# Kernel optimization log

Measured on AMD Instinct MI355X. Metric: run time of the kernel, lower is better.

Reference implementation:

```python
import jax, jax.numpy as jnp
import numpy as np

B, N, C, CD, R = 8, 16384, 32, 256, 32


def setup_inputs() -> dict:
    key = jax.random.key(0)
    ks = jax.random.split(key, 12)
    f32 = jnp.float32
    p = lambda k, shape, s=0.05: jax.random.normal(k, shape, f32) * s
    return {
        "features": jax.random.normal(ks[0], (B, C, N), f32),
        "coords": jax.random.normal(ks[1], (B, 3, N), f32),
        "condition": jax.random.normal(ks[2], (B, CD), f32),
        "conv1_w": p(ks[3], (C, C, 3, 3, 3)), "conv1_b": jnp.zeros((C,), f32),
        "gn1_g": jnp.ones((C,), f32), "gn1_b": jnp.zeros((C,), f32),
        "mod1_w": p(ks[4], (2 * C, CD)),
        "mod1_b": jnp.concatenate([jnp.ones((C,)), jnp.zeros((C,))]).astype(f32),
        "conv2_w": p(ks[5], (C, C, 3, 3, 3)), "conv2_b": jnp.zeros((C,), f32),
        "gn2_g": jnp.ones((C,), f32), "gn2_b": jnp.zeros((C,), f32),
        "mod2_w": p(ks[6], (2 * C, CD)),
        "mod2_b": jnp.concatenate([jnp.ones((C,)), jnp.zeros((C,))]).astype(f32),
        "se_w1": p(ks[7], (C // 8, C)), "se_w2": p(ks[8], (C, C // 8)),
        "pc_w": p(ks[9], (C, C)), "pc_b": jnp.zeros((C,), f32),
        "gnp_g": jnp.ones((C,), f32), "gnp_b": jnp.zeros((C,), f32),
        "modp_w": p(ks[10], (2 * C, CD)),
        "modp_b": jnp.concatenate([jnp.ones((C,)), jnp.zeros((C,))]).astype(f32),
    }


def group_norm(x, g, b, G=8, eps=1e-5):
    shape = x.shape
    xg = x.reshape(shape[0], G, -1)
    m = xg.mean(-1, keepdims=True)
    v = xg.var(-1, keepdims=True)
    xn = ((xg - m) * jax.lax.rsqrt(v + eps)).reshape(shape)
    bshape = (1, shape[1]) + (1,) * (x.ndim - 2)
    return xn * g.reshape(bshape) + b.reshape(bshape)


def adagn(x, c, g, b, mw, mb):
    # GroupNorm then scale/shift from SiLU(c) @ Linear
    x = group_norm(x, g, b)
    m = jax.nn.silu(c) @ mw.T + mb  # (B, 2C)
    scale, shift = jnp.split(m, 2, axis=1)
    bshape = (x.shape[0], x.shape[1]) + (1,) * (x.ndim - 2)
    return x * scale.reshape(bshape) + shift.reshape(bshape)


def voxelize(features, coords, r):
    # scatter-average point features into r^3 grid; coords detached as in torch
    coords = jax.lax.stop_gradient(coords)
    nc = coords - coords.mean(2, keepdims=True)
    denom = jnp.max(jnp.linalg.norm(nc, axis=1, keepdims=True), axis=2, keepdims=True) * 2.0
    nc = nc / denom + 0.5
    nc = jnp.clip(nc * r, 0, r - 1)  # (B,3,N) continuous in [0, r-1]
    vc = jnp.round(nc).astype(jnp.int32)
    idx = (vc[:, 0] * r + vc[:, 1]) * r + vc[:, 2]  # (B,N) flat voxel ids

    def per_batch(f, i):
        s = jax.ops.segment_sum(f.T, i, num_segments=r ** 3)  # (V, D)
        cnt = jax.ops.segment_sum(jnp.ones(i.shape, f.dtype), i, num_segments=r ** 3)
        return (s / jnp.maximum(cnt, 1.0)[:, None]).T.reshape(f.shape[0], r, r, r)

    vox = jax.vmap(per_batch)(features, idx)  # (B, D, r, r, r)
    return vox, nc


def devoxelize(vox, coords, r):
    # trilinear gather of voxel features back to points
    Bv, D = vox.shape[:2]
    flat = vox.reshape(Bv, D, r * r * r)
    lo = jnp.floor(coords)
    frac = coords - lo
    lo = lo.astype(jnp.int32)
    hi = jnp.minimum(lo + 1, r - 1)
    gather = jax.vmap(lambda f, i: f[:, i])  # per-batch (D,V)[:, (N,)] -> (D,N)
    out = jnp.zeros((Bv, D, coords.shape[2]), vox.dtype)
    for dx in (0, 1):
        ix = hi[:, 0] if dx else lo[:, 0]
        wx = frac[:, 0] if dx else 1.0 - frac[:, 0]
        for dy in (0, 1):
            iy = hi[:, 1] if dy else lo[:, 1]
            wy = frac[:, 1] if dy else 1.0 - frac[:, 1]
            for dz in (0, 1):
                iz = hi[:, 2] if dz else lo[:, 2]
                wz = frac[:, 2] if dz else 1.0 - frac[:, 2]
                idx = (ix * r + iy) * r + iz
                out = out + gather(flat, idx) * (wx * wy * wz)[:, None, :]
    return out


def conv3d(x, w, b):
    y = jax.lax.conv_general_dilated(x, w, (1, 1, 1), 'SAME',
                                     dimension_numbers=('NCDHW', 'OIDHW', 'NCDHW'))
    return y + b[None, :, None, None, None]


def reference(features, coords, condition, conv1_w, conv1_b, gn1_g, gn1_b, mod1_w,
              mod1_b, conv2_w, conv2_b, gn2_g, gn2_b, mod2_w, mod2_b, se_w1, se_w2,
              pc_w, pc_b, gnp_g, gnp_b, modp_w, modp_b):
    vox, nc = voxelize(features, coords, R)
    v = conv3d(vox, conv1_w, conv1_b)
    v = jax.nn.silu(adagn(v, condition, gn1_g, gn1_b, mod1_w, mod1_b))
    v = conv3d(v, conv2_w, conv2_b)
    v = adagn(v, condition, gn2_g, gn2_b, mod2_w, mod2_b)
    # SE3d squeeze-excite
    s = jax.nn.sigmoid(jax.nn.relu(v.mean((2, 3, 4)) @ se_w1.T) @ se_w2.T)
    v = v * s[:, :, None, None, None]
    vfeat = devoxelize(v, nc, R)  # (B, C, N)
    # point branch: 1x1 conv + AdaGN + SiLU
    px = jnp.einsum('bdn,od->bon', features, pc_w) + pc_b[None, :, None]
    px = jax.nn.silu(adagn(px, condition, gnp_g, gnp_b, modp_w, modp_b))
    return vfeat + px
```

## Files before the change

kernel.cpp:

```cpp
#include <hip/hip_runtime.h>
#include <math.h>

#define DEV_INLINE __device__ __forceinline__

namespace {

typedef unsigned short u16;
typedef unsigned int u32;
typedef __attribute__((ext_vector_type(8))) short short8v;
typedef __attribute__((ext_vector_type(16))) float f32x16;

constexpr int Bn = 8, Cn = 32, Nn = 16384, Rn = 32, Vn = Rn * Rn * Rn;

DEV_INLINE float siluf(float x) { return x / (1.0f + __expf(-x)); }
DEV_INLINE float bf2f(u16 u) { union { u32 i; float f; } x; x.i = (u32)u << 16; return x.f; }
DEV_INLINE u16 f2bf(float f) {
  union { float f; u32 i; } x; x.f = f;
  return (u16)((x.i + 0x7FFFu + ((x.i >> 16) & 1u)) >> 16);
}
DEV_INLINE u32 pack2(float a, float b) { return (u32)f2bf(a) | ((u32)f2bf(b) << 16); }
DEV_INLINE void unpack8(uint4 u, float* f) {
  f[0] = bf2f(u.x & 0xffff); f[1] = bf2f(u.x >> 16);
  f[2] = bf2f(u.y & 0xffff); f[3] = bf2f(u.y >> 16);
  f[4] = bf2f(u.z & 0xffff); f[5] = bf2f(u.z >> 16);
  f[6] = bf2f(u.w & 0xffff); f[7] = bf2f(u.w >> 16);
}

__global__ void k_cpart1(const float* __restrict__ coords, float* __restrict__ csum) {
  int blk = blockIdx.x;
  int b = blk >> 3, s = blk & 7;
  int t = threadIdx.x;
  const float* cb = coords + (size_t)b * 3 * Nn;
  int n0 = s * 2048;
  float sx = 0.f, sy = 0.f, sz = 0.f;
  for (int n = n0 + t; n < n0 + 2048; n += 256) {
    sx += cb[n]; sy += cb[Nn + n]; sz += cb[2 * Nn + n];
  }
  #pragma unroll
  for (int m = 1; m <= 32; m <<= 1) {
    sx += __shfl_xor(sx, m); sy += __shfl_xor(sy, m); sz += __shfl_xor(sz, m);
  }
  __shared__ float rs[3][4];
  if ((t & 63) == 0) { rs[0][t >> 6] = sx; rs[1][t >> 6] = sy; rs[2][t >> 6] = sz; }
  __syncthreads();
  if (t < 3) atomicAdd(&csum[b * 4 + t], rs[t][0] + rs[t][1] + rs[t][2] + rs[t][3]);
}

__global__ void k_cpart2(const float* __restrict__ coords, const float* __restrict__ csum,
                         int* __restrict__ cmax) {
  int blk = blockIdx.x;
  int b = blk >> 3, s = blk & 7;
  int t = threadIdx.x;
  const float* cb = coords + (size_t)b * 3 * Nn;
  const float invn = 1.0f / (float)Nn;
  float mx = csum[b * 4] * invn, my = csum[b * 4 + 1] * invn, mz = csum[b * 4 + 2] * invn;
  int n0 = s * 2048;
  float mq = 0.f;
  for (int n = n0 + t; n < n0 + 2048; n += 256) {
    float x = cb[n] - mx, y = cb[Nn + n] - my, z = cb[2 * Nn + n] - mz;
    mq = fmaxf(mq, x * x + y * y + z * z);
  }
  #pragma unroll
  for (int m = 1; m <= 32; m <<= 1) mq = fmaxf(mq, __shfl_xor(mq, m));
  __shared__ float rm[4];
  if ((t & 63) == 0) rm[t >> 6] = mq;
  __syncthreads();
  if (t == 0) {
    float v = fmaxf(fmaxf(rm[0], rm[1]), fmaxf(rm[2], rm[3]));
    atomicMax(cmax + b, __float_as_int(v));
  }
}

__global__ void k_cfinal(const float* __restrict__ coords, const float* __restrict__ csum,
                         const int* __restrict__ cmax, float* __restrict__ nc,
                         int* __restrict__ vidx, int* __restrict__ hist) {
  int i = blockIdx.x * 256 + threadIdx.x;
  int b = i >> 14, n = i & (Nn - 1);
  const float* cb = coords + (size_t)b * 3 * Nn;
  const float invn = 1.0f / (float)Nn;
  float mx = csum[b * 4] * invn, my = csum[b * 4 + 1] * invn, mz = csum[b * 4 + 2] * invn;
  float inv = 1.0f / (2.0f * sqrtf(__int_as_float(cmax[b])));
  float x = (cb[n] - mx) * inv + 0.5f;
  float y = (cb[Nn + n] - my) * inv + 0.5f;
  float z = (cb[2 * Nn + n] - mz) * inv + 0.5f;
  x = fminf(fmaxf(x * (float)Rn, 0.f), (float)(Rn - 1));
  y = fminf(fmaxf(y * (float)Rn, 0.f), (float)(Rn - 1));
  z = fminf(fmaxf(z * (float)Rn, 0.f), (float)(Rn - 1));
  float* ncb = nc + (size_t)b * 3 * Nn;
  ncb[n] = x; ncb[Nn + n] = y; ncb[2 * Nn + n] = z;
  int vx = (int)rintf(x), vy = (int)rintf(y), vz = (int)rintf(z);
  int v = (vx * Rn + vy) * Rn + vz;
  vidx[i] = v;
  atomicAdd(&hist[b * Vn + v], 1);
}

__global__ __launch_bounds__(256, 2) void k_pxlin(
    const float* __restrict__ feat, const float* __restrict__ w,
    const float* __restrict__ bias, float* __restrict__ featT,
    u16* __restrict__ pxb) {
  __shared__ float lw[1024];
  __shared__ float lb[32];
  __shared__ float lbuf[256 * 33];
  int t = threadIdx.x;
  for (int i = t; i < 1024; i += 256) lw[i] = w[i];
  if (t < 32) lb[t] = bias[t];
  int blk = blockIdx.x;
  int b = blk >> 6, tile = blk & 63;
  int n0 = tile * 256, n = n0 + t;
  float fr[32];
  const float* fb = feat + (size_t)b * 32 * Nn + n;
  #pragma unroll
  for (int ci = 0; ci < 32; ++ci) {
    fr[ci] = fb[(size_t)ci * Nn];
    lbuf[t * 33 + ci] = fr[ci];
  }
  __syncthreads();
  float* ftb = featT + ((size_t)b * Nn + n0) * 32;
  #pragma unroll
  for (int j = 0; j < 32; ++j) {
    int idx = j * 256 + t;
    ftb[idx] = lbuf[(idx >> 5) * 33 + (idx & 31)];
  }
  __syncthreads();
  u32* lbu = reinterpret_cast<u32*>(lbuf);
  #pragma unroll
  for (int p2 = 0; p2 < 16; ++p2) {
    int co0 = p2 * 2;
    float a0 = lb[co0], a1 = lb[co0 + 1];
    #pragma unroll
    for (int ci = 0; ci < 32; ++ci) {
      a0 += lw[co0 * 32 + ci] * fr[ci];
      a1 += lw[(co0 + 1) * 32 + ci] * fr[ci];
    }
    lbu[t * 17 + p2] = pack2(a0, a1);
  }
  __syncthreads();
  u32* pxu = reinterpret_cast<u32*>(pxb) + ((size_t)b * Nn + n0) * 16;
  #pragma unroll
  for (int j = 0; j < 16; ++j) {
    int idx = j * 256 + t;
    pxu[idx] = lbu[(idx >> 4) * 17 + (idx & 15)];
  }
}

__global__ void k_scan1(const int* __restrict__ hist, int* __restrict__ offs,
                        int* __restrict__ bsum) {
  __shared__ int sd[256];
  int t = threadIdx.x, blk = blockIdx.x;
  int4 h = reinterpret_cast<const int4*>(hist)[blk * 256 + t];
  int s = h.x + h.y + h.z + h.w;
  sd[t] = s; __syncthreads();
  for (int off = 1; off < 256; off <<= 1) {
    int add = (t >= off) ? sd[t - off] : 0;
    __syncthreads();
    sd[t] += add;
    __syncthreads();
  }
  int excl = sd[t] - s;
  int4 o;
  o.x = excl; o.y = excl + h.x; o.z = o.y + h.y; o.w = o.z + h.z;
  reinterpret_cast<int4*>(offs)[blk * 256 + t] = o;
  if (t == 0) bsum[blk] = sd[255];
}

__global__ void k_scan2(const int* __restrict__ bsum, int* __restrict__ bbase) {
  __shared__ int sd[256];
  int t = threadIdx.x;
  int s = bsum[t];
  sd[t] = s; __syncthreads();
  for (int off = 1; off < 256; off <<= 1) {
    int add = (t >= off) ? sd[t - off] : 0;
    __syncthreads();
    sd[t] += add;
    __syncthreads();
  }
  bbase[t] = sd[t] - s;
}

__global__ void k_sortidx(const int* __restrict__ vidx, int* __restrict__ offs,
                          const int* __restrict__ bbase, int* __restrict__ pidx) {
  int i = blockIdx.x * 256 + threadIdx.x;
  int b = i >> 14, n = i & (Nn - 1);
  int g = b * Vn + vidx[i];
  int p = atomicAdd(&offs[g], 1) + bbase[g >> 10];
  pidx[p] = n;
}

__global__ void k_voxavg(const int* __restrict__ hist, const int* __restrict__ offs,
                         const int* __restrict__ bbase, const int* __restrict__ pidx,
                         const float* __restrict__ featT, uint2* __restrict__ vox0) {
  int t = threadIdx.x;
  int wv = blockIdx.x * 4 + (t >> 6);
  int lane = t & 63;
  int c4 = lane & 7, j = lane >> 3;
  int b = wv >> 15;
  int cnt = hist[wv];
  float ax = 0.f, ay = 0.f, az = 0.f, aw = 0.f;
  if (cnt > 0) {
    int end = offs[wv] + bbase[wv >> 10];
    int start = end - cnt;
    const float4* ft = reinterpret_cast<const float4*>(featT) + (size_t)b * Nn * 8;
    for (int k = start + j; k < end; k += 8) {
      int n = pidx[k];
      float4 v = ft[n * 8 + c4];
      ax += v.x; ay += v.y; az += v.z; aw += v.w;
    }
    #pragma unroll
    for (int m = 8; m <= 32; m <<= 1) {
      ax += __shfl_xor(ax, m); ay += __shfl_xor(ay, m);
      az += __shfl_xor(az, m); aw += __shfl_xor(aw, m);
    }
    float invc = 1.0f / (float)cnt;
    ax *= invc; ay *= invc; az *= invc; aw *= invc;
  }
  if (j == 0) {
    uint2 o;
    o.x = pack2(ax, ay);
    o.y = pack2(az, aw);
    vox0[(size_t)wv * 8 + c4] = o;
  }
}

__global__ void k_twz(const float* __restrict__ w, u16* __restrict__ wt) {
  int i = blockIdx.x * 256 + threadIdx.x;
  if (i >= 27 * 32 * 32) return;
  int e = i & 7, l = (i >> 3) & 63, h = (i >> 9) & 1, k = i >> 10;
  int co = l & 31, ci = h * 16 + ((l >> 5) << 3) + e;
  wt[i] = f2bf(w[(co * 32 + ci) * 27 + k]);
}

__global__ void k_mods(const float* __restrict__ cond,
                       const float* __restrict__ w1, const float* __restrict__ b1,
                       const float* __restrict__ w2, const float* __restrict__ b2,
                       const float* __restrict__ wp, const float* __restrict__ bp,
                       float* __restrict__ m1, float* __restrict__ m2,
                       float* __restrict__ mp) {
  int blk = blockIdx.x;
  int mat = blk >> 3, b = blk & 7;
  int t = threadIdx.x;
  __shared__ float sc[256];
  sc[t] = siluf(cond[b * 256 + t]);
  __syncthreads();
  const float* w = (mat == 0) ? w1 : ((mat == 1) ? w2 : wp);
  const float* bb = (mat == 0) ? b1 : ((mat == 1) ? b2 : bp);
  float* dst = (mat == 0) ? m1 : ((mat == 1) ? m2 : mp);
  int wave = t >> 6, lane = t & 63;
  const float4* w4 = reinterpret_cast<const float4*>(w);
  float4 sv = reinterpret_cast<const float4*>(sc)[lane];
  #pragma unroll
  for (int i = 0; i < 16; ++i) {
    int oo = wave * 16 + i;
    float4 wv = w4[oo * 64 + lane];
    float p = wv.x * sv.x + wv.y * sv.y + wv.z * sv.z + wv.w * sv.w;
    #pragma unroll
    for (int m = 1; m <= 32; m <<= 1) p += __shfl_xor(p, m);
    if (lane == 0) dst[b * 64 + oo] = p + bb[oo];
  }
}

template <bool AFF>
__global__ __launch_bounds__(512, 4) void k_conv(
    const u16* __restrict__ in, const u16* __restrict__ wt,
    const float* __restrict__ bias, const float* __restrict__ Ac,
    const float* __restrict__ Bc, u16* __restrict__ out,
    float* __restrict__ pstat) {
  __shared__ uint4 lds_x4[4096];
  int t = threadIdx.x;
  int blk = blockIdx.x;
  int yp = blk & 3, x = (blk >> 2) & 31, b = blk >> 7;
  int y0 = yp * 8;
  size_t bbase = (size_t)b * Vn;

  for (int i = t; i < 4080; i += 512) {
    int col = i / 136, rem = i - col * 136;
    int c4 = rem / 34, r = rem - c4 * 34;
    int dxp = col / 10, yy = col - dxp * 10;
    int gx = x + dxp - 1, gy = y0 + yy - 1, z = r - 1;
    uint4 val = make_uint4(0u, 0u, 0u, 0u);
    if (gx >= 0 && gx < 32 && (unsigned)gy < 32u && (unsigned)z < 32u) {
      val = *reinterpret_cast<const uint4*>(
          in + (bbase + (size_t)((gx * 32 + gy) * 32 + z)) * 32 + c4 * 8);
      if (AFF) {
        float f[8];
        unpack8(val, f);
        float4 A0 = reinterpret_cast<const float4*>(Ac)[b * 8 + c4 * 2];
        float4 A1 = reinterpret_cast<const float4*>(Ac)[b * 8 + c4 * 2 + 1];
        float4 B0 = reinterpret_cast<const float4*>(Bc)[b * 8 + c4 * 2];
        float4 B1 = reinterpret_cast<const float4*>(Bc)[b * 8 + c4 * 2 + 1];
        f[0] = siluf(f[0] * A0.x + B0.x); f[1] = siluf(f[1] * A0.y + B0.y);
        f[2] = siluf(f[2] * A0.z + B0.z); f[3] = siluf(f[3] * A0.w + B0.w);
        f[4] = siluf(f[4] * A1.x + B1.x); f[5] = siluf(f[5] * A1.y + B1.y);
        f[6] = siluf(f[6] * A1.z + B1.z); f[7] = siluf(f[7] * A1.w + B1.w);
        val.x = pack2(f[0], f[1]); val.y = pack2(f[2], f[3]);
        val.z = pack2(f[4], f[5]); val.w = pack2(f[6], f[7]);
      }
    }
    lds_x4[i] = val;
  }
  __syncthreads();

  int w = t >> 6, lane = t & 63;
  int zc = lane & 31, hi = lane >> 5;
  int y = y0 + w;

  f32x16 acc;
  #pragma unroll
  for (int q = 0; q < 4; ++q) {
    float4 bq = *reinterpret_cast<const float4*>(bias + q * 8 + hi * 4);
    acc[q * 4 + 0] = bq.x; acc[q * 4 + 1] = bq.y;
    acc[q * 4 + 2] = bq.z; acc[q * 4 + 3] = bq.w;
  }

  const u16* lx = reinterpret_cast<const u16*>(lds_x4);
  const u16* gw = wt + lane * 8;

  #pragma unroll
  for (int dxp = 0; dxp < 3; ++dxp) {
    #pragma unroll
    for (int dyp = 0; dyp < 3; ++dyp) {
      int col = dxp * 10 + w + dyp;
      #pragma unroll
      for (int dzp = 0; dzp < 3; ++dzp) {
        int k = (dxp * 3 + dyp) * 3 + dzp;
        short8v a0 = *reinterpret_cast<const short8v*>(gw + (k * 2 + 0) * 512);
        short8v a1 = *reinterpret_cast<const short8v*>(gw + (k * 2 + 1) * 512);
        short8v b0 = *reinterpret_cast<const short8v*>(
            lx + ((col * 4 + hi) * 34 + zc + dzp) * 8);
        short8v b1 = *reinterpret_cast<const short8v*>(
            lx + ((col * 4 + 2 + hi) * 34 + zc + dzp) * 8);
        acc = __builtin_amdgcn_mfma_f32_32x32x16_bf16(a0, b0, acc, 0, 0, 0);
        acc = __builtin_amdgcn_mfma_f32_32x32x16_bf16(a1, b1, acc, 0, 0, 0);
      }
    }
  }

  size_t off = (bbase + (size_t)((x * 32 + y) * 32 + zc)) * 32;
  #pragma unroll
  for (int q = 0; q < 4; ++q) {
    uint2 o;
    o.x = pack2(acc[q * 4 + 0], acc[q * 4 + 1]);
    o.y = pack2(acc[q * 4 + 2], acc[q * 4 + 3]);
    *reinterpret_cast<uint2*>(out + off + q * 8 + hi * 4) = o;
  }

  float s16[16], q16[16];
  #pragma unroll
  for (int r = 0; r < 16; ++r) { s16[r] = acc[r]; q16[r] = acc[r] * acc[r]; }
  #pragma unroll
  for (int m = 1; m <= 16; m <<= 1) {
    #pragma unroll
    for (int r = 0; r < 16; ++r) {
      s16[r] += __shfl_xor(s16[r], m);
      q16[r] += __shfl_xor(q16[r], m);
    }
  }
  __syncthreads();
  float* sred = reinterpret_cast<float*>(lds_x4);
  if ((lane & 31) == 0) {
    #pragma unroll
    for (int r = 0; r < 16; ++r) {
      int co = (r & 3) + 8 * (r >> 2) + 4 * hi;
      sred[w * 64 + co] = s16[r];
      sred[512 + w * 64 + co] = q16[r];
    }
  }
  __syncthreads();
  if (t < 64) {
    int arr = t >> 5, c = t & 31;
    const float* bp_ = sred + arr * 512 + c;
    float v = bp_[0] + bp_[64] + bp_[128] + bp_[192] +
              bp_[256] + bp_[320] + bp_[384] + bp_[448];
    pstat[blk * 64 + arr * 32 + c] = v;
  }
}

__global__ void k_statspx(const u16* __restrict__ x, float* __restrict__ psum,
                          float* __restrict__ psq, int segs) {
  int blk = blockIdx.x;
  int b = blk / segs;
  int t = threadIdx.x;
  int c8 = t & 3, vsub = t >> 2;
  float s[8], q[8];
  #pragma unroll
  for (int j = 0; j < 8; ++j) { s[j] = 0.f; q[j] = 0.f; }
  const uint4* xb = reinterpret_cast<const uint4*>(x) + (size_t)blk * 4096;
  for (int it = 0; it < 16; ++it) {
    int v = it * 64 + vsub;
    uint4 u = xb[v * 4 + c8];
    float f[8];
    unpack8(u, f);
    #pragma unroll
    for (int j = 0; j < 8; ++j) { s[j] += f[j]; q[j] += f[j] * f[j]; }
  }
  #pragma unroll
  for (int m = 4; m <= 32; m <<= 1) {
    #pragma unroll
    for (int j = 0; j < 8; ++j) {
      s[j] += __shfl_xor(s[j], m);
      q[j] += __shfl_xor(q[j], m);
    }
  }
  __shared__ float ls[2][4][4][8];
  int wv = t >> 6;
  if ((t & 63) < 4) {
    #pragma unroll
    for (int j = 0; j < 8; ++j) { ls[0][wv][c8][j] = s[j]; ls[1][wv][c8][j] = q[j]; }
  }
  __syncthreads();
  if (t < 64) {
    int arr = t >> 5, c = t & 31;
    float v = ls[arr][0][c >> 3][c & 7] + ls[arr][1][c >> 3][c & 7] +
              ls[arr][2][c >> 3][c & 7] + ls[arr][3][c >> 3][c & 7];
    atomicAdd((arr == 0 ? psum : psq) + b * 32 + c, v);
  }
}

__global__ void k_coef1(const float* __restrict__ pstat, const float* __restrict__ mod,
                        const float* __restrict__ g, const float* __restrict__ bgn,
                        float* __restrict__ A, float* __restrict__ Bc) {
  int t = threadIdx.x;
  int b = t >> 5, c = t & 31;
  float cs = 0.f, cq = 0.f;
  const float* p = pstat + (size_t)b * 128 * 64;
  for (int i = 0; i < 128; ++i) {
    cs += p[i * 64 + c];
    cq += p[i * 64 + 32 + c];
  }
  __shared__ float ls[256], lq[256];
  ls[t] = cs; lq[t] = cq;
  __syncthreads();
  int gb = t & ~3;
  float s4 = ls[gb] + ls[gb + 1] + ls[gb + 2] + ls[gb + 3];
  float q4 = lq[gb] + lq[gb + 1] + lq[gb + 2] + lq[gb + 3];
  const float cntf = 4.0f * (float)Vn;
  float mean = s4 / cntf;
  float var = q4 / cntf - mean * mean;
  float rstd = rsqrtf(var + 1e-5f);
  float scale = mod[b * 64 + c], shift = mod[b * 64 + 32 + c];
  A[t] = rstd * g[c] * scale;
  Bc[t] = (bgn[c] - mean * rstd * g[c]) * scale + shift;
}

__global__ void k_coef2(const float* __restrict__ pstat, const float* __restrict__ mod,
                        const float* __restrict__ g, const float* __restrict__ bgn,
                        const float* __restrict__ sw1, const float* __restrict__ sw2,
                        float* __restrict__ S, float* __restrict__ T) {
  __shared__ float zm[8][32];
  __shared__ float hh[8][4];
  __shared__ float ls[256], lq[256];
  int t = threadIdx.x;
  int b = t >> 5, c = t & 31;
  float cs = 0.f, cq = 0.f;
  const float* p = pstat + (size_t)b * 128 * 64;
  for (int i = 0; i < 128; ++i) {
    cs += p[i * 64 + c];
    cq += p[i * 64 + 32 + c];
  }
  ls[t] = cs; lq[t] = cq;
  __syncthreads();
  int gb = t & ~3;
  float s4 = ls[gb] + ls[gb + 1] + ls[gb + 2] + ls[gb + 3];
  float q4 = lq[gb] + lq[gb + 1] + lq[gb + 2] + lq[gb + 3];
  const float cntf = 4.0f * (float)Vn;
  float mean = s4 / cntf;
  float var = q4 / cntf - mean * mean;
  float rstd = rsqrtf(var + 1e-5f);
  float scale = mod[b * 64 + c], shift = mod[b * 64 + 32 + c];
  float A = rstd * g[c] * scale;
  float Bv = (bgn[c] - mean * rstd * g[c]) * scale + shift;
  float chmean = cs / (float)Vn;
  zm[b][c] = A * chmean + Bv;
  __syncthreads();
  if (t < 32) {
    int b2 = t >> 2, j = t & 3;
    float h = 0;
    for (int cc = 0; cc < 32; ++cc) h += sw1[j * 32 + cc] * zm[b2][cc];
    hh[b2][j] = fmaxf(h, 0.f);
  }
  __syncthreads();
  float sig = 0;
  for (int j = 0; j < 4; ++j) sig += sw2[c * 4 + j] * hh[b][j];
  sig = 1.0f / (1.0f + __expf(-sig));
  S[t] = A * sig;
  T[t] = Bv * sig;
}

__global__ void k_coefp(const float* __restrict__ psum, const float* __restrict__ psq,
                        const float* __restrict__ mod, const float* __restrict__ g,
                        const float* __restrict__ bgn, float* __restrict__ A,
                        float* __restrict__ Bc) {
  __shared__ float ls[256], lq[256];
  int t = threadIdx.x;
  int b = t >> 5, c = t & 31;
  ls[t] = psum[t]; lq[t] = psq[t];
  __syncthreads();
  int gb = t & ~3;
  float s4 = ls[gb] + ls[gb + 1] + ls[gb + 2] + ls[gb + 3];
  float q4 = lq[gb] + lq[gb + 1] + lq[gb + 2] + lq[gb + 3];
  const float cntf = 4.0f * (float)Nn;
  float m = s4 / cntf;
  float var = q4 / cntf - m * m;
  float r = rsqrtf(var + 1e-5f);
  float scale = mod[b * 64 + c], shift = mod[b * 64 + 32 + c];
  A[t] = r * g[c] * scale;
  Bc[t] = (bgn[c] - m * r * g[c]) * scale + shift;
}

__global__ void k_devoxfinal(const u16* __restrict__ vox, const float* __restrict__ nc,
                             const u16* __restrict__ pxb, const float* __restrict__ S,
                             const float* __restrict__ T, const float* __restrict__ Ap,
                             const float* __restrict__ Bp, float* __restrict__ out) {
  int i = blockIdx.x * 256 + threadIdx.x;
  int b = i >> 14, n = i & (Nn - 1);
  const float* ncb = nc + (size_t)b * 3 * Nn;
  float fx = ncb[n], fy = ncb[Nn + n], fz = ncb[2 * Nn + n];
  float lxf = floorf(fx), lyf = floorf(fy), lzf = floorf(fz);
  float wx1 = fx - lxf, wy1 = fy - lyf, wz1 = fz - lzf;
  int lx = (int)lxf, ly = (int)lyf, lz = (int)lzf;
  int hx = min(lx + 1, 31), hy = min(ly + 1, 31), hz = min(lz + 1, 31);
  float a[32];
  #pragma unroll
  for (int c = 0; c < 32; ++c) a[c] = 0.f;
  for (int corner = 0; corner < 8; ++corner) {
    int cx = (corner & 4) ? hx : lx;
    int cy = (corner & 2) ? hy : ly;
    int cz = (corner & 1) ? hz : lz;
    float ww = ((corner & 4) ? wx1 : 1.f - wx1) *
               ((corner & 2) ? wy1 : 1.f - wy1) *
               ((corner & 1) ? wz1 : 1.f - wz1);
    const uint4* p = reinterpret_cast<const uint4*>(
        vox + ((size_t)b * Vn + (size_t)((cx * 32 + cy) * 32 + cz)) * 32);
    #pragma unroll
    for (int qq = 0; qq < 4; ++qq) {
      float f[8];
      unpack8(p[qq], f);
      #pragma unroll
      for (int j = 0; j < 8; ++j) a[qq * 8 + j] += ww * f[j];
    }
  }
  const uint4* pp = reinterpret_cast<const uint4*>(pxb) + (size_t)i * 4;
  float* o = out + (size_t)b * 32 * Nn + n;
  #pragma unroll
  for (int qq = 0; qq < 4; ++qq) {
    float pf[8];
    unpack8(pp[qq], pf);
    #pragma unroll
    for (int j = 0; j < 8; ++j) {
      int c = qq * 8 + j;
      float y = pf[j] * Ap[b * 32 + c] + Bp[b * 32 + c];
      o[(size_t)c * Nn] = a[c] * S[b * 32 + c] + T[b * 32 + c] + siluf(y);
    }
  }
}

}

extern "C" void kernel_launch(void* const* d_in, const int* in_sizes, int n_in,
                              void* d_out, int out_size, void* d_ws, size_t ws_size,
                              hipStream_t stream) {
  (void)in_sizes; (void)n_in; (void)out_size; (void)ws_size;
  const float* features = (const float*)d_in[0];
  const float* coords = (const float*)d_in[1];
  const float* condition = (const float*)d_in[2];
  const float* conv1_w = (const float*)d_in[3];
  const float* conv1_b = (const float*)d_in[4];
  const float* gn1_g = (const float*)d_in[5];
  const float* gn1_b = (const float*)d_in[6];
  const float* mod1_w = (const float*)d_in[7];
  const float* mod1_b = (const float*)d_in[8];
  const float* conv2_w = (const float*)d_in[9];
  const float* conv2_b = (const float*)d_in[10];
  const float* gn2_g = (const float*)d_in[11];
  const float* gn2_b = (const float*)d_in[12];
  const float* mod2_w = (const float*)d_in[13];
  const float* mod2_b = (const float*)d_in[14];
  const float* se_w1 = (const float*)d_in[15];
  const float* se_w2 = (const float*)d_in[16];
  const float* pc_w = (const float*)d_in[17];
  const float* pc_b = (const float*)d_in[18];
  const float* gnp_g = (const float*)d_in[19];
  const float* gnp_b = (const float*)d_in[20];
  const float* modp_w = (const float*)d_in[21];
  const float* modp_b = (const float*)d_in[22];

  char* w = (char*)d_ws;
  float* featT = (float*)w;
  u16* vox1 = (u16*)w;
  w += 16777216;
  u16* vox2 = (u16*)w; w += 16777216;
  u16* vox0 = (u16*)w; w += 16777216;
  u16* pxb = (u16*)w;  w += 8388608;
  int* hist = (int*)w;  w += 1048576;
  float* psump = (float*)w; w += 1024;
  float* psqp = (float*)w;  w += 1024;
  float* csum = (float*)w;  w += 128;
  int* cmax = (int*)w;      w += 64;
  int* offs = (int*)w;  w += 1048576;
  int* bsum = (int*)w;  w += 1024;
  int* bbase = (int*)w; w += 1024;
  int* pidx = (int*)w;  w += 524288;
  float* ncb = (float*)w;   w += 1572864;
  int* vidx = (int*)w;      w += 524288;
  u16* wt1b = (u16*)w;      w += 55296;
  u16* wt2b = (u16*)w;      w += 55296;
  float* pstat1 = (float*)w; w += 262144;
  float* pstat2 = (float*)w; w += 262144;
  float* m1 = (float*)w;    w += 2048;
  float* m2 = (float*)w;    w += 2048;
  float* mp = (float*)w;    w += 2048;
  float* A1 = (float*)w;    w += 1024;
  float* B1 = (float*)w;    w += 1024;
  float* Sc = (float*)w;    w += 1024;
  float* Tc = (float*)w;    w += 1024;
  float* Ap = (float*)w;    w += 1024;
  float* Bp = (float*)w;    w += 1024;
  float* out = (float*)d_out;

  hipMemsetAsync(hist, 0, 1048576 + 1024 + 1024 + 128 + 64, stream);

  k_pxlin<<<Bn * 64, 256, 0, stream>>>(features, pc_w, pc_b, featT, pxb);
  k_cpart1<<<Bn * 8, 256, 0, stream>>>(coords, csum);
  k_twz<<<108, 256, 0, stream>>>(conv1_w, wt1b);
  k_twz<<<108, 256, 0, stream>>>(conv2_w, wt2b);
  k_mods<<<24, 256, 0, stream>>>(condition, mod1_w, mod1_b, mod2_w, mod2_b,
                                 modp_w, modp_b, m1, m2, mp);
  k_statspx<<<Bn * 16, 256, 0, stream>>>(pxb, psump, psqp, 16);
  k_coefp<<<1, 256, 0, stream>>>(psump, psqp, mp, gnp_g, gnp_b, Ap, Bp);
  k_cpart2<<<Bn * 8, 256, 0, stream>>>(coords, csum, cmax);
  k_cfinal<<<(Bn * Nn) / 256, 256, 0, stream>>>(coords, csum, cmax, ncb, vidx, hist);
  k_scan1<<<256, 256, 0, stream>>>(hist, offs, bsum);
  k_scan2<<<1, 256, 0, stream>>>(bsum, bbase);
  k_sortidx<<<(Bn * Nn) / 256, 256, 0, stream>>>(vidx, offs, bbase, pidx);
  k_voxavg<<<(Bn * Vn) / 4, 256, 0, stream>>>(hist, offs, bbase, pidx, featT,
                                              (uint2*)vox0);
  k_conv<false><<<1024, 512, 0, stream>>>(vox0, wt1b, conv1_b, nullptr, nullptr,
                                          vox1, pstat1);
  k_coef1<<<1, 256, 0, stream>>>(pstat1, m1, gn1_g, gn1_b, A1, B1);
  k_conv<true><<<1024, 512, 0, stream>>>(vox1, wt2b, conv2_b, A1, B1, vox2, pstat2);
  k_coef2<<<1, 256, 0, stream>>>(pstat2, m2, gn2_g, gn2_b, se_w1, se_w2, Sc, Tc);
  k_devoxfinal<<<(Bn * Nn) / 256, 256, 0, stream>>>(vox2, ncb, pxb, Sc, Tc, Ap, Bp, out);
}
```

Before: 222.1 us.

## Make conv3d blocks persistent over y-tiles with double-buffered LDS and register weights

Each conv block now handles a whole x-slice (8 y-tiles of 4 rows) instead of one 8-row tile. The next tile's halo is prefetched into registers and written into a second LDS buffer while MFMAs run on the current one. Weights are held in registers for the whole block, and the input-channel halves are split across wave pairs, then reduced through LDS. This cuts redundant halo loads and per-tile weight reloads, but leaves only 256 blocks (a single wave of blocks on the GPU), raises register pressure, and adds an LDS reduction and extra barriers per tile.

New measurement: 217.3 us. -2.2%, faster.

```diff
diff --git a/kernel.cpp b/kernel.cpp
--- a/kernel.cpp
+++ b/kernel.cpp
@@ -259,117 +259,160 @@
 }
 
 template <bool AFF>
-__global__ __launch_bounds__(512, 4) void k_conv(
+DEV_INLINE void stage_load(const u16* __restrict__ in, size_t bbase, int x, int ytn,
+                           int t, const float* __restrict__ Ac,
+                           const float* __restrict__ Bc, int b, uint4* sv) {
+  #pragma unroll
+  for (int it = 0; it < 5; ++it) {
+    int i = it * 512 + t;
+    uint4 val = make_uint4(0u, 0u, 0u, 0u);
+    if (i < 2448) {
+      int col = i / 136, rem = i - col * 136;
+      int c4 = rem / 34, r = rem - c4 * 34;
+      int dxp = col / 6, yy = col - dxp * 6;
+      int gx = x + dxp - 1, gy = ytn * 4 + yy - 1, z = r - 1;
+      if ((unsigned)gx < 32u && (unsigned)gy < 32u && (unsigned)z < 32u) {
+        val = *reinterpret_cast<const uint4*>(
+            in + (bbase + (size_t)((gx * 32 + gy) * 32 + z)) * 32 + c4 * 8);
+        if (AFF) {
+          float f[8];
+          unpack8(val, f);
+          float4 A0 = reinterpret_cast<const float4*>(Ac)[b * 8 + c4 * 2];
+          float4 A1 = reinterpret_cast<const float4*>(Ac)[b * 8 + c4 * 2 + 1];
+          float4 B0 = reinterpret_cast<const float4*>(Bc)[b * 8 + c4 * 2];
+          float4 B1 = reinterpret_cast<const float4*>(Bc)[b * 8 + c4 * 2 + 1];
+          f[0] = siluf(f[0] * A0.x + B0.x); f[1] = siluf(f[1] * A0.y + B0.y);
+          f[2] = siluf(f[2] * A0.z + B0.z); f[3] = siluf(f[3] * A0.w + B0.w);
+          f[4] = siluf(f[4] * A1.x + B1.x); f[5] = siluf(f[5] * A1.y + B1.y);
+          f[6] = siluf(f[6] * A1.z + B1.z); f[7] = siluf(f[7] * A1.w + B1.w);
+          val.x = pack2(f[0], f[1]); val.y = pack2(f[2], f[3]);
+          val.z = pack2(f[4], f[5]); val.w = pack2(f[6], f[7]);
+        }
+      }
+    }
+    sv[it] = val;
+  }
+}
+
+DEV_INLINE void stage_store(uint4* __restrict__ dst, int t, const uint4* sv) {
+  #pragma unroll
+  for (int it = 0; it < 5; ++it) {
+    int i = it * 512 + t;
+    if (i < 2448) dst[i] = sv[it];
+  }
+}
+
+template <bool AFF>
+__global__ __launch_bounds__(512, 2) void k_conv(
     const u16* __restrict__ in, const u16* __restrict__ wt,
     const float* __restrict__ bias, const float* __restrict__ Ac,
     const float* __restrict__ Bc, u16* __restrict__ out,
     float* __restrict__ pstat) {
-  __shared__ uint4 lds_x4[4096];
+  __shared__ uint4 lds_x[4896];
+  __shared__ float red[4096];
   int t = threadIdx.x;
   int blk = blockIdx.x;
-  int yp = blk & 3, x = (blk >> 2) & 31, b = blk >> 7;
-  int y0 = yp * 8;
+  int x = blk & 31, b = blk >> 5;
   size_t bbase = (size_t)b * Vn;
-
-  for (int i = t; i < 4080; i += 512) {
-    int col = i / 136, rem = i - col * 136;
-    int c4 = rem / 34, r = rem - c4 * 34;
-    int dxp = col / 10, yy = col - dxp * 10;
-    int gx = x + dxp - 1, gy = y0 + yy - 1, z = r - 1;
-    uint4 val = make_uint4(0u, 0u, 0u, 0u);
-    if (gx >= 0 && gx < 32 && (unsigned)gy < 32u && (unsigned)z < 32u) {
-      val = *reinterpret_cast<const uint4*>(
-          in + (bbase + (size_t)((gx * 32 + gy) * 32 + z)) * 32 + c4 * 8);
-      if (AFF) {
-        float f[8];
-        unpack8(val, f);
-        float4 A0 = reinterpret_cast<const float4*>(Ac)[b * 8 + c4 * 2];
-        float4 A1 = reinterpret_cast<const float4*>(Ac)[b * 8 + c4 * 2 + 1];
-        float4 B0 = reinterpret_cast<const float4*>(Bc)[b * 8 + c4 * 2];
-        float4 B1 = reinterpret_cast<const float4*>(Bc)[b * 8 + c4 * 2 + 1];
-        f[0] = siluf(f[0] * A0.x + B0.x); f[1] = siluf(f[1] * A0.y + B0.y);
-        f[2] = siluf(f[2] * A0.z + B0.z); f[3] = siluf(f[3] * A0.w + B0.w);
-        f[4] = siluf(f[4] * A1.x + B1.x); f[5] = siluf(f[5] * A1.y + B1.y);
-        f[6] = siluf(f[6] * A1.z + B1.z); f[7] = siluf(f[7] * A1.w + B1.w);
-        val.x = pack2(f[0], f[1]); val.y = pack2(f[2], f[3]);
-        val.z = pack2(f[4], f[5]); val.w = pack2(f[6], f[7]);
+  int w = t >> 6, lane = t & 63;
+  int ys = w >> 1, h = w & 1;
+  int zc = lane & 31, hi = lane >> 5;
+
+  short8v wreg[27];
+  #pragma unroll
+  for (int k = 0; k < 27; ++k)
+    wreg[k] = *reinterpret_cast<const short8v*>(wt + ((size_t)(k * 2 + h) * 64 + lane) * 8);
+
+  uint4 sv[5];
+  stage_load<AFF>(in, bbase, x, 0, t, Ac, Bc, b, sv);
+  stage_store(lds_x, t, sv);
+  __syncthreads();
+
+  float s16[16], q16[16];
+  #pragma unroll
+  for (int r = 0; r < 16; ++r) { s16[r] = 0.f; q16[r] = 0.f; }
+
+  int cur = 0;
+  for (int yt = 0; yt < 8; ++yt) {
+    if (yt < 7) stage_load<AFF>(in, bbase, x, yt + 1, t, Ac, Bc, b, sv);
+
+    f32x16 acc;
+    #pragma unroll
+    for (int r = 0; r < 16; ++r) acc[r] = 0.f;
+    if (h == 0) {
+      #pragma unroll
+      for (int q = 0; q < 4; ++q) {
+        float4 bq = *reinterpret_cast<const float4*>(bias + q * 8 + hi * 4);
+        acc[q * 4 + 0] = bq.x; acc[q * 4 + 1] = bq.y;
+        acc[q * 4 + 2] = bq.z; acc[q * 4 + 3] = bq.w;
       }
     }
-    lds_x4[i] = val;
-  }
-  __syncthreads();
-
-  int w = t >> 6, lane = t & 63;
-  int zc = lane & 31, hi = lane >> 5;
-  int y = y0 + w;
-
-  f32x16 acc;
-  #pragma unroll
-  for (int q = 0; q < 4; ++q) {
-    float4 bq = *reinterpret_cast<const float4*>(bias + q * 8 + hi * 4);
-    acc[q * 4 + 0] = bq.x; acc[q * 4 + 1] = bq.y;
-    acc[q * 4 + 2] = bq.z; acc[q * 4 + 3] = bq.w;
-  }
-
-  const u16* lx = reinterpret_cast<const u16*>(lds_x4);
-  const u16* gw = wt + lane * 8;
-
-  #pragma unroll
-  for (int dxp = 0; dxp < 3; ++dxp) {
-    #pragma unroll
-    for (int dyp = 0; dyp < 3; ++dyp) {
-      int col = dxp * 10 + w + dyp;
-      #pragma unroll
-      for (int dzp = 0; dzp < 3; ++dzp) {
-        int k = (dxp * 3 + dyp) * 3 + dzp;
-        short8v a0 = *reinterpret_cast<const short8v*>(gw + (k * 2 + 0) * 512);
-        short8v a1 = *reinterpret_cast<const short8v*>(gw + (k * 2 + 1) * 512);
-        short8v b0 = *reinterpret_cast<const short8v*>(
-            lx + ((col * 4 + hi) * 34 + zc + dzp) * 8);
-        short8v b1 = *reinterpret_cast<const short8v*>(
-            lx + ((col * 4 + 2 + hi) * 34 + zc + dzp) * 8);
-        acc = __builtin_amdgcn_mfma_f32_32x32x16_bf16(a0, b0, acc, 0, 0, 0);
-        acc = __builtin_amdgcn_mfma_f32_32x32x16_bf16(a1, b1, acc, 0, 0, 0);
+
+    const u16* lx = reinterpret_cast<const u16*>(lds_x + cur * 2448);
+    int cbase = 2 * h + hi;
+    #pragma unroll
+    for (int dxp = 0; dxp < 3; ++dxp) {
+      #pragma unroll
+      for (int dyp = 0; dyp < 3; ++dyp) {
+        int col = dxp * 6 + ys + dyp;
+        const u16* lcol = lx + ((col * 4 + cbase) * 34 + zc) * 8;
+        #pragma unroll
+        for (int dzp = 0; dzp < 3; ++dzp) {
+          int k = (dxp * 3 + dyp) * 3 + dzp;
+          short8v bb = *reinterpret_cast<const short8v*>(lcol + dzp * 8);
+          acc = __builtin_amdgcn_mfma_f32_32x32x16_bf16(wreg[k], bb, acc, 0, 0, 0);
+        }
       }
     }
-  }
-
-  size_t off = (bbase + (size_t)((x * 32 + y) * 32 + zc)) * 32;
-  #pragma unroll
-  for (int q = 0; q < 4; ++q) {
-    uint2 o;
-    o.x = pack2(acc[q * 4 + 0], acc[q * 4 + 1]);
-    o.y = pack2(acc[q * 4 + 2], acc[q * 4 + 3]);
-    *reinterpret_cast<uint2*>(out + off + q * 8 + hi * 4) = o;
-  }
-
-  float s16[16], q16[16];
-  #pragma unroll
-  for (int r = 0; r < 16; ++r) { s16[r] = acc[r]; q16[r] = acc[r] * acc[r]; }
-  #pragma unroll
-  for (int m = 1; m <= 16; m <<= 1) {
-    #pragma unroll
-    for (int r = 0; r < 16; ++r) {
-      s16[r] += __shfl_xor(s16[r], m);
-      q16[r] += __shfl_xor(q16[r], m);
-    }
-  }
-  __syncthreads();
-  float* sred = reinterpret_cast<float*>(lds_x4);
-  if ((lane & 31) == 0) {
-    #pragma unroll
-    for (int r = 0; r < 16; ++r) {
-      int co = (r & 3) + 8 * (r >> 2) + 4 * hi;
-      sred[w * 64 + co] = s16[r];
-      sred[512 + w * 64 + co] = q16[r];
+
+    if (h == 1) {
+      #pragma unroll
+      for (int r = 0; r < 16; ++r) red[ys * 1024 + r * 64 + lane] = acc[r];
+    }
+    __syncthreads();
+    if (h == 0) {
+      #pragma unroll
+      for (int r = 0; r < 16; ++r) acc[r] += red[ys * 1024 + r * 64 + lane];
+      int y = yt * 4 + ys;
+      size_t off = (bbase + (size_t)((x * 32 + y) * 32 + zc)) * 32;
+      #pragma unroll
+      for (int q = 0; q < 4; ++q) {
+        uint2 o;
+        o.x = pack2(acc[q * 4 + 0], acc[q * 4 + 1]);
+        o.y = pack2(acc[q * 4 + 2], acc[q * 4 + 3]);
+        *reinterpret_cast<uint2*>(out + off + q * 8 + hi * 4) = o;
+      }
+      #pragma unroll
+      for (int r = 0; r < 16; ++r) { s16[r] += acc[r]; q16[r] += acc[r] * acc[r]; }
+    }
+    if (yt < 7) stage_store(lds_x + (cur ^ 1) * 2448, t, sv);
+    __syncthreads();
+    cur ^= 1;
+  }
+
+  if (h == 0) {
+    #pragma unroll
+    for (int m = 1; m <= 16; m <<= 1) {
+      #pragma unroll
+      for (int r = 0; r < 16; ++r) {
+        s16[r] += __shfl_xor(s16[r], m);
+        q16[r] += __shfl_xor(q16[r], m);
+      }
+    }
+    if ((lane & 31) == 0) {
+      #pragma unroll
+      for (int r = 0; r < 16; ++r) {
+        int co = (r & 3) + 8 * (r >> 2) + 4 * hi;
+        red[ys * 64 + co] = s16[r];
+        red[256 + ys * 64 + co] = q16[r];
+      }
     }
   }
   __syncthreads();
   if (t < 64) {
     int arr = t >> 5, c = t & 31;
-    const float* bp_ = sred + arr * 512 + c;
-    float v = bp_[0] + bp_[64] + bp_[128] + bp_[192] +
-              bp_[256] + bp_[320] + bp_[384] + bp_[448];
+    const float* pr = red + arr * 256 + c;
+    float v = pr[0] + pr[64] + pr[128] + pr[192];
     pstat[blk * 64 + arr * 32 + c] = v;
   }
 }
@@ -421,8 +464,8 @@
   int t = threadIdx.x;
   int b = t >> 5, c = t & 31;
   float cs = 0.f, cq = 0.f;
-  const float* p = pstat + (size_t)b * 128 * 64;
-  for (int i = 0; i < 128; ++i) {
+  const float* p = pstat + (size_t)b * 32 * 64;
+  for (int i = 0; i < 32; ++i) {
     cs += p[i * 64 + c];
     cq += p[i * 64 + 32 + c];
   }
@@ -451,8 +494,8 @@
   int t = threadIdx.x;
   int b = t >> 5, c = t & 31;
   float cs = 0.f, cq = 0.f;
-  const float* p = pstat + (size_t)b * 128 * 64;
-  for (int i = 0; i < 128; ++i) {
+  const float* p = pstat + (size_t)b * 32 * 64;
+  for (int i = 0; i < 32; ++i) {
     cs += p[i * 64 + c];
     cq += p[i * 64 + 32 + c];
   }
@@ -473,9 +516,9 @@
   __syncthreads();
   if (t < 32) {
     int b2 = t >> 2, j = t & 3;
-    float h = 0;
-    for (int cc = 0; cc < 32; ++cc) h += sw1[j * 32 + cc] * zm[b2][cc];
-    hh[b2][j] = fmaxf(h, 0.f);
+    float hsum = 0;
+    for (int cc = 0; cc < 32; ++cc) hsum += sw1[j * 32 + cc] * zm[b2][cc];
+    hh[b2][j] = fmaxf(hsum, 0.f);
   }
   __syncthreads();
   float sig = 0;
@@ -603,8 +646,8 @@
   int* vidx = (int*)w;      w += 524288;
   u16* wt1b = (u16*)w;      w += 55296;
   u16* wt2b = (u16*)w;      w += 55296;
-  float* pstat1 = (float*)w; w += 262144;
-  float* pstat2 = (float*)w; w += 262144;
+  float* pstat1 = (float*)w; w += 65536;
+  float* pstat2 = (float*)w; w += 65536;
   float* m1 = (float*)w;    w += 2048;
   float* m2 = (float*)w;    w += 2048;
   float* mp = (float*)w;    w += 2048;
@@ -633,10 +676,10 @@
   k_sortidx<<<(Bn * Nn) / 256, 256, 0, stream>>>(vidx, offs, bbase, pidx);
   k_voxavg<<<(Bn * Vn) / 4, 256, 0, stream>>>(hist, offs, bbase, pidx, featT,
                                               (uint2*)vox0);
-  k_conv<false><<<1024, 512, 0, stream>>>(vox0, wt1b, conv1_b, nullptr, nullptr,
-                                          vox1, pstat1);
+  k_conv<false><<<256, 512, 0, stream>>>(vox0, wt1b, conv1_b, nullptr, nullptr,
+                                         vox1, pstat1);
   k_coef1<<<1, 256, 0, stream>>>(pstat1, m1, gn1_g, gn1_b, A1, B1);
-  k_conv<true><<<1024, 512, 0, stream>>>(vox1, wt2b, conv2_b, A1, B1, vox2, pstat2);
+  k_conv<true><<<256, 512, 0, stream>>>(vox1, wt2b, conv2_b, A1, B1, vox2, pstat2);
   k_coef2<<<1, 256, 0, stream>>>(pstat2, m2, gn2_g, gn2_b, se_w1, se_w2, Sc, Tc);
   k_devoxfinal<<<(Bn * Nn) / 256, 256, 0, stream>>>(vox2, ncb, pxb, Sc, Tc, Ap, Bp, out);
 }
```
